# Kernel optimization log

Hardware: AMD Instinct MI355X
Metric: run time of the kernel (lower is better)

The kernel has to match this reference:

```python
import jax, jax.numpy as jnp
import numpy as np

# MORRConfig_20um_MQ ring parameters
A = 0.8578   # attenuation factor a
R = 0.8985   # coupling factor r

IN_C, OUT_C, KS, STRIDE, PAD, MB = 32, 64, 3, 1, 1, 8
WIN = IN_C * KS * KS                      # 288 = kernel_size^2 * in_channel
WIN_PAD = ((WIN + MB - 1) // MB) * MB     # padded to multiple of miniblock
OUT_PAD = ((OUT_C + MB - 1) // MB) * MB
Q = WIN_PAD // MB                         # grid_dim_x = 36
P = OUT_PAD // MB                         # grid_dim_y = 8
MORR_GAIN = (100.0 / (WIN // MB)) ** 0.5  # input power normalization


def mrr_tr(phi):
    # all-pass MORR roundtrip-phase -> transmission intensity
    # T = (a^2 - 2ar cos(phi) + r^2) / (1 - 2ar cos(phi) + (ar)^2)
    c = 2.0 * A * R * jnp.cos(phi)
    return (A * A + R * R - c) / (1.0 + (A * R) ** 2 - c)


def im2col(x):
    # torch F.unfold ordering: feature dim ordered (C, ki, kj)
    B, C, H, W = x.shape
    xp = jnp.pad(x, ((0, 0), (0, 0), (PAD, PAD), (PAD, PAD)))
    Ho = (H + 2 * PAD - KS) // STRIDE + 1
    Wo = (W + 2 * PAD - KS) // STRIDE + 1
    cols = [xp[:, :, i:i + Ho * STRIDE:STRIDE, j:j + Wo * STRIDE:STRIDE]
            for i in range(KS) for j in range(KS)]
    p = jnp.stack(cols, axis=2)               # [B, C, KS*KS, Ho, Wo]
    return p.reshape(B, C * KS * KS, Ho * Wo), Ho, Wo


def setup_inputs() -> dict:
    key = jax.random.key(0)
    k1, k2, k3 = jax.random.split(key, 3)
    x = jax.random.uniform(k1, (8, IN_C, 64, 64), dtype=jnp.float32)  # intensity-encoded, nonneg
    weight = jax.random.uniform(k2, (P, Q, MB), dtype=jnp.float32) * 0.2  # nonneg MORR weights
    morr_output_scale = jax.random.normal(k3, (max(1, Q // 2) + 1,), dtype=jnp.float32) * 0.1
    return {"x": x, "weight": weight, "morr_output_scale": morr_output_scale}


def reference(x, weight, morr_output_scale):
    B = x.shape[0]
    cols, Ho, Wo = im2col(x)
    xb = cols.transpose(0, 2, 1)
    if WIN_PAD > WIN:
        xb = jnp.pad(xb, ((0, 0), (0, 0), (0, WIN_PAD - WIN)))
    xb = xb.reshape(-1, Q, MB)                # [Bs, Q, MB]
    inten = (xb * xb) * MORR_GAIN             # optical intensity (power-normalized)

    # block-circulant weighted phase accumulation == circular conv per (p,q) block, via rFFT
    Wf = jnp.fft.rfft(weight, axis=-1)        # [P, Q, MBf]
    Xf = jnp.fft.rfft(inten, axis=-1)         # [Bs, Q, MBf]
    phase = jnp.fft.irfft(Xf[:, None, :, :] * Wf[None], n=MB, axis=-1)  # [Bs, P, Q, MB]

    tr = mrr_tr(phase)                        # MORR nonlinear transfer

    # differential rails: learnable balancing factor per block-column pair (+1 pad scale)
    half = morr_output_scale[:-1]             # [Q//2]
    if Q % 2 == 0:
        scale = jnp.concatenate([half, -half])                              # [Q]
    else:
        scale = jnp.concatenate([half, morr_output_scale[-1:], -half])      # [Q]

    out = jnp.einsum("bpqk,q->bpk", tr, scale).reshape(-1, OUT_PAD)[:, :OUT_C]
    out = out.reshape(B, Ho * Wo, OUT_C).transpose(0, 2, 1).reshape(B, OUT_C, Ho, Wo)
    return out
```

## Files before the change

### kernel.cpp

```cpp
#include <hip/hip_runtime.h>

#define THREADS 512

#define IN_C 32
#define OUT_C 64
#define HW 64
#define Q_N 36
#define P_N 8
#define MB 8

#define SXW 66
#define SXPL (3 * SXW)
#define SXSZ (IN_C * SXPL)

__global__ __launch_bounds__(THREADS, 4)
void morr_conv_kernel(const float* __restrict__ x,
                      const float* __restrict__ weight,
                      const float* __restrict__ mos,
                      float* __restrict__ out)
{
    __shared__ float sx[SXSZ];
    __shared__ float slds[Q_N];

    const int tid = threadIdx.x;
    const int blk = blockIdx.x;
    const int b   = blk >> 6;
    const int row = blk & 63;

    const float GI = 1.6666666666666667f * 0.15915494309189535f;

    const float A_ = 0.8578f, R_ = 0.8985f;
    const float S_ = A_ * A_ + R_ * R_;
    const float D_ = 1.f + (A_ * R_) * (A_ * R_);
    const float C2 = 2.f * A_ * R_;
    const float E_ = S_ - D_;

    for (int idx = tid; idx < SXSZ; idx += THREADS) {
        int c    = idx / SXPL;
        int rem  = idx - c * SXPL;
        int r    = rem / SXW;
        int col  = rem - r * SXW;
        int gh = row + r - 1;
        int gw = col - 1;
        float v = 0.f;
        if ((unsigned)gh < 64u && (unsigned)gw < 64u)
            v = x[((b * IN_C + c) * HW + gh) * HW + gw];
        sx[idx] = GI * v * v;
    }
    if (tid < Q_N)
        slds[tid] = ((tid < 18) ? mos[tid] : -mos[tid - 18]) * E_;
    __syncthreads();

    const int px = tid & 63;
    const int p  = __builtin_amdgcn_readfirstlane(tid >> 6);
    const float* __restrict__ wp = weight + p * (Q_N * MB);

    float acc[8];
#pragma unroll
    for (int i = 0; i < 8; ++i) acc[i] = 0.f;

#pragma unroll 1
    for (int z = 0; z < 4; ++z) {
        const int sbase = (z * 8) * SXPL + px;
        const int qz = z * 9;
        const float* __restrict__ wpz = wp + z * 9 * MB;
#pragma unroll
        for (int qi = 0; qi < 9; ++qi) {
            float iv[8];
#pragma unroll
            for (int j = 0; j < 8; ++j) {
                const int u  = qi * 8 + j;
                const int cu = u / 9;
                const int r  = u - cu * 9;
                const int ki = r / 3;
                const int kj = r - ki * 3;
                iv[j] = sx[sbase + cu * SXPL + ki * SXW + kj];
            }
            float wv[8];
#pragma unroll
            for (int m = 0; m < 8; ++m) wv[m] = wpz[qi * MB + m];

            float ph[8];
#pragma unroll
            for (int k = 0; k < 8; ++k) ph[k] = iv[0] * wv[k];
#pragma unroll
            for (int j = 1; j < 8; ++j) {
#pragma unroll
                for (int k = 0; k < 8; ++k)
                    ph[k] = fmaf(iv[j], wv[(k - j) & 7], ph[k]);
            }
            const float sc = slds[qz + qi];
#pragma unroll
            for (int k = 0; k < 8; ++k) {
                float cc = __builtin_amdgcn_cosf(ph[k]);
                float d  = fmaf(-C2, cc, D_);
                acc[k] = fmaf(sc, __builtin_amdgcn_rcpf(d), acc[k]);
            }
        }
    }

    float* op = out + ((b * OUT_C + p * MB) * (HW * HW)) + row * HW + px;
#pragma unroll
    for (int k = 0; k < 8; ++k)
        op[k * (HW * HW)] = acc[k];
}

extern "C" void kernel_launch(void* const* d_in, const int* in_sizes, int n_in,
                              void* d_out, int out_size, void* d_ws, size_t ws_size,
                              hipStream_t stream) {
    const float* x      = (const float*)d_in[0];
    const float* weight = (const float*)d_in[1];
    const float* mos    = (const float*)d_in[2];
    float* out = (float*)d_out;

    dim3 grid(512), block(THREADS);
    hipLaunchKernelGGL(morr_conv_kernel, grid, block, 0, stream, x, weight, mos, out);
}
```

Measured before the change: 92.97 us.

## Compute circulant phase products with bf16 MFMA instead of scalar FMAs

The per-block circulant convolution becomes a bf16 matrix multiply on the 16x16x32 MFMA instruction. Inputs are laid out in LDS as a per-pixel im2col, weights are expanded into circulant form, and lanes outside the active K slice read a zero buffer. This removes the 64 scalar FMAs per block but lowers the phase precision to bf16 before the cosine, and the LDS footprint grows to about 75KB, which limits how many blocks fit per CU.

```diff
diff --git a/kernel.cpp b/kernel.cpp
--- a/kernel.cpp
+++ b/kernel.cpp
@@ -3,15 +3,23 @@
 #define THREADS 512
 
 #define IN_C 32
-#define OUT_C 64
 #define HW 64
 #define Q_N 36
-#define P_N 8
-#define MB 8
 
-#define SXW 66
-#define SXPL (3 * SXW)
-#define SXSZ (IN_C * SXPL)
+typedef float f32x4 __attribute__((ext_vector_type(4)));
+typedef short s16x8 __attribute__((ext_vector_type(8)));
+
+#define AIM_OFF 0
+#define WB_OFF  37888
+#define ZB_OFF  74752
+#define SC_OFF  75264
+#define LDS_BYTES 75424
+
+__device__ __forceinline__ unsigned short f2bf(float f) {
+    union { float f; unsigned int u; } v; v.f = f;
+    unsigned int t = v.u + 0x7FFFu + ((v.u >> 16) & 1u);
+    return (unsigned short)(t >> 16);
+}
 
 __global__ __launch_bounds__(THREADS, 4)
 void morr_conv_kernel(const float* __restrict__ x,
@@ -19,8 +27,10 @@
                       const float* __restrict__ mos,
                       float* __restrict__ out)
 {
-    __shared__ float sx[SXSZ];
-    __shared__ float slds[Q_N];
+    __shared__ __align__(16) unsigned char lds[LDS_BYTES];
+    unsigned short* Aim = (unsigned short*)(lds + AIM_OFF);
+    unsigned short* Wb  = (unsigned short*)(lds + WB_OFF);
+    float* scl          = (float*)(lds + SC_OFF);
 
     const int tid = threadIdx.x;
     const int blk = blockIdx.x;
@@ -28,81 +38,93 @@
     const int row = blk & 63;
 
     const float GI = 1.6666666666666667f * 0.15915494309189535f;
-
     const float A_ = 0.8578f, R_ = 0.8985f;
     const float S_ = A_ * A_ + R_ * R_;
     const float D_ = 1.f + (A_ * R_) * (A_ * R_);
     const float C2 = 2.f * A_ * R_;
     const float E_ = S_ - D_;
 
-    for (int idx = tid; idx < SXSZ; idx += THREADS) {
-        int c    = idx / SXPL;
-        int rem  = idx - c * SXPL;
-        int r    = rem / SXW;
-        int col  = rem - r * SXW;
-        int gh = row + r - 1;
-        int gw = col - 1;
-        float v = 0.f;
-        if ((unsigned)gh < 64u && (unsigned)gw < 64u)
-            v = x[((b * IN_C + c) * HW + gh) * HW + gw];
-        sx[idx] = GI * v * v;
+    {
+        const int px = tid & 63;
+        const int g  = tid >> 6;
+#pragma unroll
+        for (int c2 = 0; c2 < 4; ++c2) {
+            const int c = g * 4 + c2;
+            const float* xc = x + ((b * IN_C + c) * HW) * HW;
+#pragma unroll
+            for (int ki = 0; ki < 3; ++ki) {
+                const int gh = row + ki - 1;
+                const bool rok = (unsigned)gh < 64u;
+#pragma unroll
+                for (int kj = 0; kj < 3; ++kj) {
+                    const int gw = px + kj - 1;
+                    float v = (rok && (unsigned)gw < 64u) ? xc[gh * HW + gw] : 0.f;
+                    Aim[px * 296 + c * 9 + ki * 3 + kj] = f2bf(GI * v * v);
+                }
+            }
+        }
     }
-    if (tid < Q_N)
-        slds[tid] = ((tid < 18) ? mos[tid] : -mos[tid - 18]) * E_;
+#pragma unroll
+    for (int i = 0; i < 36; ++i) {
+        const int idx = tid + 512 * i;
+        const int q  = idx >> 9;
+        const int mt = (idx >> 7) & 3;
+        const int pr = (idx >> 3) & 15;
+        const int j  = idx & 7;
+        const int pk = mt * 16 + pr;
+        const int p  = pk >> 3, k = pk & 7;
+        Wb[idx] = f2bf(weight[p * 288 + q * 8 + ((k - j) & 7)]);
+    }
+    if (tid < 256) ((unsigned short*)(lds + ZB_OFF))[tid] = 0;
+    if (tid < Q_N) scl[tid] = ((tid < 18) ? mos[tid] : -mos[tid - 18]) * E_;
     __syncthreads();
 
-    const int px = tid & 63;
-    const int p  = __builtin_amdgcn_readfirstlane(tid >> 6);
-    const float* __restrict__ wp = weight + p * (Q_N * MB);
+    const int wv = tid >> 6;
+    const int l  = tid & 63;
+    const int ll = l & 15;
+    const int lh = l >> 4;
+    const int nt = wv & 3;
+    const int m0 = (wv >> 2) * 2;
+
+    const unsigned short* bB = Aim + (nt * 16 + ll) * 296;
+    const unsigned short* aW = (l < 16)
+        ? (Wb + (m0 * 16 + ll) * 8)
+        : (const unsigned short*)(lds + ZB_OFF);
+    const int qstep = (l < 16) ? 512 : 0;
 
     float acc[8];
 #pragma unroll
     for (int i = 0; i < 8; ++i) acc[i] = 0.f;
 
-#pragma unroll 1
-    for (int z = 0; z < 4; ++z) {
-        const int sbase = (z * 8) * SXPL + px;
-        const int qz = z * 9;
-        const float* __restrict__ wpz = wp + z * 9 * MB;
+    const f32x4 cz = {0.f, 0.f, 0.f, 0.f};
+
 #pragma unroll
-        for (int qi = 0; qi < 9; ++qi) {
-            float iv[8];
+    for (int q = 0; q < Q_N; ++q) {
+        s16x8 bfrag = *(const s16x8*)(bB + q * 8);
+        s16x8 a0 = *(const s16x8*)(aW);
+        s16x8 a1 = *(const s16x8*)(aW + 128);
+        f32x4 d0 = __builtin_amdgcn_mfma_f32_16x16x32_bf16(a0, bfrag, cz, 0, 0, 0);
+        f32x4 d1 = __builtin_amdgcn_mfma_f32_16x16x32_bf16(a1, bfrag, cz, 0, 0, 0);
+        const float sc = scl[q];
 #pragma unroll
-            for (int j = 0; j < 8; ++j) {
-                const int u  = qi * 8 + j;
-                const int cu = u / 9;
-                const int r  = u - cu * 9;
-                const int ki = r / 3;
-                const int kj = r - ki * 3;
-                iv[j] = sx[sbase + cu * SXPL + ki * SXW + kj];
-            }
-            float wv[8];
+        for (int r = 0; r < 4; ++r) {
+            float c0 = __builtin_amdgcn_cosf(d0[r]);
+            acc[r]     = fmaf(sc, __builtin_amdgcn_rcpf(fmaf(-C2, c0, D_)), acc[r]);
+            float c1 = __builtin_amdgcn_cosf(d1[r]);
+            acc[4 + r] = fmaf(sc, __builtin_amdgcn_rcpf(fmaf(-C2, c1, D_)), acc[4 + r]);
+        }
+        aW += qstep;
+    }
+
+    const int col = nt * 16 + ll;
 #pragma unroll
-            for (int m = 0; m < 8; ++m) wv[m] = wpz[qi * MB + m];
-
-            float ph[8];
+    for (int t = 0; t < 2; ++t) {
 #pragma unroll
-            for (int k = 0; k < 8; ++k) ph[k] = iv[0] * wv[k];
-#pragma unroll
-            for (int j = 1; j < 8; ++j) {
-#pragma unroll
-                for (int k = 0; k < 8; ++k)
-                    ph[k] = fmaf(iv[j], wv[(k - j) & 7], ph[k]);
-            }
-            const float sc = slds[qz + qi];
-#pragma unroll
-            for (int k = 0; k < 8; ++k) {
-                float cc = __builtin_amdgcn_cosf(ph[k]);
-                float d  = fmaf(-C2, cc, D_);
-                acc[k] = fmaf(sc, __builtin_amdgcn_rcpf(d), acc[k]);
-            }
+        for (int r = 0; r < 4; ++r) {
+            const int pk = (m0 + t) * 16 + lh * 4 + r;
+            out[(b * 64 + pk) * (HW * HW) + row * HW + col] = acc[t * 4 + r];
         }
     }
-
-    float* op = out + ((b * OUT_C + p * MB) * (HW * HW)) + row * HW + px;
-#pragma unroll
-    for (int k = 0; k < 8; ++k)
-        op[k * (HW * HW)] = acc[k];
 }
 
 extern "C" void kernel_launch(void* const* d_in, const int* in_sizes, int n_in,
```

After: 86.06 us. 1.08x faster.
